# Optimization experiments

Hardware: AMD Instinct MI355X
Metric: run time of the kernel (lower is better)

Reference implementation:

```python
import jax, jax.numpy as jnp
import numpy as np
import math

B, S, HID = 1, 2048, 4096
NH, NKV, HD = 32, 8, 128
ROPE_THETA = 500000.0
NEG = -1e9

def _rope_tables(seq_len, head_dim, theta):
    inv_freq = 1.0 / (theta ** (np.arange(0, head_dim, 2, dtype=np.float32) / head_dim))
    t = np.arange(seq_len, dtype=np.float32)
    freqs = np.outer(t, inv_freq)                      # [S, HD/2]
    emb = np.concatenate([freqs, freqs], axis=-1)      # [S, HD]
    return jnp.asarray(np.cos(emb))[None], jnp.asarray(np.sin(emb))[None]  # [1,S,HD]

def setup_inputs() -> dict:
    key = jax.random.key(0)
    ks = jax.random.split(key, 6)
    hidden_states = jax.random.normal(ks[0], (B, S, HID), jnp.float32)
    # causal additive mask [B,1,S,S]
    causal = jnp.triu(jnp.full((S, S), NEG, jnp.float32), k=1)
    attention_mask = jnp.broadcast_to(causal, (B, 1, S, S))
    cos, sin = _rope_tables(S, HD, ROPE_THETA)
    sc = 0.02
    wq = jax.random.normal(ks[1], (NH * HD, HID), jnp.float32) * sc
    wk = jax.random.normal(ks[2], (NKV * HD, HID), jnp.float32) * sc
    wv = jax.random.normal(ks[3], (NKV * HD, HID), jnp.float32) * sc
    wo = jax.random.normal(ks[4], (HID, NH * HD), jnp.float32) * sc
    return {"hidden_states": hidden_states, "attention_mask": attention_mask,
            "cos": cos, "sin": sin, "wq": wq, "wk": wk, "wv": wv, "wo": wo}

def _rotate_half(x):
    x1, x2 = jnp.split(x, 2, axis=-1)
    return jnp.concatenate([-x2, x1], axis=-1)

def reference(hidden_states, attention_mask, cos, sin, wq, wk, wv, wo):
    b, s, _ = hidden_states.shape
    # QKV projections (torch Linear: x @ W^T)
    q = jnp.einsum('bsm,nm->bsn', hidden_states, wq).reshape(b, s, NH, HD).transpose(0, 2, 1, 3)
    k = jnp.einsum('bsm,nm->bsn', hidden_states, wk).reshape(b, s, NKV, HD).transpose(0, 2, 1, 3)
    v = jnp.einsum('bsm,nm->bsn', hidden_states, wv).reshape(b, s, NKV, HD).transpose(0, 2, 1, 3)
    # RoPE (cos/sin broadcast over heads via unsqueeze dim 1)
    c = cos[:, None, :, :]
    sn = sin[:, None, :, :]
    q = q * c + _rotate_half(q) * sn
    k = k * c + _rotate_half(k) * sn
    # GQA: repeat kv heads
    n_rep = NH // NKV
    k = jnp.repeat(k, n_rep, axis=1)
    v = jnp.repeat(v, n_rep, axis=1)
    scores = jnp.einsum('bhqd,bhkd->bhqk', q, k) / math.sqrt(HD)
    scores = scores + attention_mask[:, :, :, :s]
    attn = jax.nn.softmax(scores.astype(jnp.float32), axis=-1).astype(q.dtype)
    out = jnp.einsum('bhqk,bhkd->bhqd', attn, v)        # [b,NH,s,HD]
    out = out.transpose(0, 2, 1, 3).reshape(b, s, NH * HD)
    return jnp.einsum('bsn,mn->bsm', out, wo)
```

## Files before the change

### kernel.cpp

```cpp
#include <hip/hip_runtime.h>
#include <hip/hip_bf16.h>
#include <stdint.h>

typedef __hip_bfloat16 bf16;
using bf16x8 = __attribute__((ext_vector_type(8))) short;
using f32x4  = __attribute__((ext_vector_type(4))) float;

#define MFMA16(a, b, c) __builtin_amdgcn_mfma_f32_16x16x32_bf16(a, b, c, 0, 0, 0)

#define S_LEN 2048
#define HID   4096
#define NH    32
#define NKV   8
#define HD    128
#define DQ    4096
#define DKV   1024
#define QK_SCALE 0.1275228868824805f

__device__ inline void gl_lds16(const bf16* g, bf16* l) {
    __builtin_amdgcn_global_load_lds(
        (const __attribute__((address_space(1))) void*)g,
        (__attribute__((address_space(3))) void*)l, 16, 0, 0);
}

__device__ inline void cvt_store4(const float* src, bf16* dst, size_t i4) {
    float4 v = ((const float4*)src)[i4];
    union { ushort4 u; bf16 h[4]; } pk;
    pk.h[0] = __float2bfloat16(v.x);
    pk.h[1] = __float2bfloat16(v.y);
    pk.h[2] = __float2bfloat16(v.z);
    pk.h[3] = __float2bfloat16(v.w);
    ((ushort4*)dst)[i4] = pk.u;
}

__global__ void conv_all(const float* __restrict__ hidden, const float* __restrict__ wq,
                         const float* __restrict__ wk, const float* __restrict__ wv,
                         bf16* __restrict__ hb, bf16* __restrict__ wqd,
                         bf16* __restrict__ wkd, bf16* __restrict__ wvd) {
    const size_t M1 = 1024 * 1024;
#pragma unroll
    for (int j = 0; j < 4; ++j) {
        size_t idx = (size_t)blockIdx.x * 1024 + j * 256 + threadIdx.x;
        if (idx < 2 * M1)      cvt_store4(hidden, hb,  idx);
        else if (idx < 6 * M1) cvt_store4(wq,     wqd, idx - 2 * M1);
        else if (idx < 7 * M1) cvt_store4(wk,     wkd, idx - 6 * M1);
        else                   cvt_store4(wv,     wvd, idx - 7 * M1);
    }
}

__global__ void conv_wo(const float* __restrict__ wo, bf16* __restrict__ wod) {
#pragma unroll
    for (int j = 0; j < 4; ++j) {
        size_t idx = (size_t)blockIdx.x * 1024 + j * 256 + threadIdx.x;
        cvt_store4(wo, wod, idx);
    }
}

__global__ void __launch_bounds__(256, 2)
qkv_gemm(const bf16* __restrict__ A, const bf16* __restrict__ Bq,
         const bf16* __restrict__ Bk, const bf16* __restrict__ Bv,
         bf16* __restrict__ Cq, bf16* __restrict__ Ck, bf16* __restrict__ Cv) {
    __shared__ __align__(16) bf16 As[128][64];
    __shared__ __align__(16) bf16 Bs[128][64];

    const int bx = blockIdx.x;
    int mode, bn;
    const bf16* B;
    if (bx < 32)      { mode = 0; B = Bq; bn = bx * 128; }
    else if (bx < 40) { mode = 1; B = Bk; bn = (bx - 32) * 128; }
    else              { mode = 2; B = Bv; bn = (bx - 40) * 128; }

    const int tid  = threadIdx.x;
    const int bm   = blockIdx.y * 128;
    const int wave = tid >> 6, lane = tid & 63;
    const int quad = lane >> 4, l15 = lane & 15;
    const int wr   = (wave >> 1) * 64;
    const int wc   = (wave & 1) * 64;

    f32x4 acc[4][4] = {};

    for (int k0 = 0; k0 < HID; k0 += 64) {
#pragma unroll
        for (int i = 0; i < 4; ++i) {
            int idx  = tid + i * 256;
            int r    = idx >> 3;
            int slot = idx & 7;
            int c    = ((slot - r) & 7) * 8;
            gl_lds16(&A[(size_t)(bm + r) * HID + k0 + c], &As[r][slot * 8]);
            gl_lds16(&B[(size_t)(bn + r) * HID + k0 + c], &Bs[r][slot * 8]);
        }
        __syncthreads();
#pragma unroll
        for (int kk = 0; kk < 64; kk += 32) {
            bf16x8 a[4], b[4];
#pragma unroll
            for (int i = 0; i < 4; ++i) {
                int row = wr + i * 16 + l15;
                a[i] = *(const bf16x8*)(&As[row][(((kk >> 3) + quad + row) & 7) * 8]);
            }
#pragma unroll
            for (int i = 0; i < 4; ++i) {
                int row = wc + i * 16 + l15;
                b[i] = *(const bf16x8*)(&Bs[row][(((kk >> 3) + quad + row) & 7) * 8]);
            }
#pragma unroll
            for (int mi = 0; mi < 4; ++mi)
#pragma unroll
                for (int ni = 0; ni < 4; ++ni)
                    acc[mi][ni] = MFMA16(a[mi], b[ni], acc[mi][ni]);
        }
        __syncthreads();
    }

    if (mode == 0) {
#pragma unroll
        for (int mi = 0; mi < 4; ++mi)
#pragma unroll
            for (int ni = 0; ni < 4; ++ni)
#pragma unroll
                for (int r = 0; r < 4; ++r)
                    Cq[(size_t)(bm + wr + mi * 16 + quad * 4 + r) * DQ +
                       bn + wc + ni * 16 + l15] = __float2bfloat16(acc[mi][ni][r]);
    } else if (mode == 1) {
#pragma unroll
        for (int mi = 0; mi < 4; ++mi)
#pragma unroll
            for (int ni = 0; ni < 4; ++ni)
#pragma unroll
                for (int r = 0; r < 4; ++r)
                    Ck[(size_t)(bm + wr + mi * 16 + quad * 4 + r) * DKV +
                       bn + wc + ni * 16 + l15] = __float2bfloat16(acc[mi][ni][r]);
    } else {
#pragma unroll
        for (int mi = 0; mi < 4; ++mi)
#pragma unroll
            for (int ni = 0; ni < 4; ++ni) {
                int row0 = bm + wr + mi * 16 + quad * 4;
                int col  = bn + wc + ni * 16 + l15;
                union { ushort4 u; bf16 h[4]; } pk;
#pragma unroll
                for (int r = 0; r < 4; ++r) pk.h[r] = __float2bfloat16(acc[mi][ni][r]);
                *(ushort4*)(&Cv[(size_t)col * S_LEN + row0]) = pk.u;
            }
    }
}

__global__ void __launch_bounds__(256, 2)
out_gemm(const bf16* __restrict__ A, const bf16* __restrict__ B,
         float* __restrict__ C) {
    __shared__ __align__(16) bf16 As[128][64];
    __shared__ __align__(16) bf16 Bs[128][64];

    const int tid  = threadIdx.x;
    const int bm   = blockIdx.y * 128;
    const int bn   = blockIdx.x * 128;
    const int wave = tid >> 6, lane = tid & 63;
    const int quad = lane >> 4, l15 = lane & 15;
    const int wr   = (wave >> 1) * 64;
    const int wc   = (wave & 1) * 64;

    f32x4 acc[4][4] = {};

    for (int k0 = 0; k0 < DQ; k0 += 64) {
#pragma unroll
        for (int i = 0; i < 4; ++i) {
            int idx  = tid + i * 256;
            int r    = idx >> 3;
            int slot = idx & 7;
            int c    = ((slot - r) & 7) * 8;
            gl_lds16(&A[(size_t)(bm + r) * DQ + k0 + c], &As[r][slot * 8]);
            gl_lds16(&B[(size_t)(bn + r) * DQ + k0 + c], &Bs[r][slot * 8]);
        }
        __syncthreads();
#pragma unroll
        for (int kk = 0; kk < 64; kk += 32) {
            bf16x8 a[4], b[4];
#pragma unroll
            for (int i = 0; i < 4; ++i) {
                int row = wr + i * 16 + l15;
                a[i] = *(const bf16x8*)(&As[row][(((kk >> 3) + quad + row) & 7) * 8]);
            }
#pragma unroll
            for (int i = 0; i < 4; ++i) {
                int row = wc + i * 16 + l15;
                b[i] = *(const bf16x8*)(&Bs[row][(((kk >> 3) + quad + row) & 7) * 8]);
            }
#pragma unroll
            for (int mi = 0; mi < 4; ++mi)
#pragma unroll
                for (int ni = 0; ni < 4; ++ni)
                    acc[mi][ni] = MFMA16(a[mi], b[ni], acc[mi][ni]);
        }
        __syncthreads();
    }

#pragma unroll
    for (int mi = 0; mi < 4; ++mi)
#pragma unroll
        for (int ni = 0; ni < 4; ++ni)
#pragma unroll
            for (int r = 0; r < 4; ++r)
                C[(size_t)(bm + wr + mi * 16 + quad * 4 + r) * HID +
                  bn + wc + ni * 16 + l15] = acc[mi][ni][r];
}

__global__ void rope_all(bf16* __restrict__ q, bf16* __restrict__ k,
                         const float* __restrict__ cosb, const float* __restrict__ sinb) {
    int idx = blockIdx.x * 256 + threadIdx.x;
    const int nq = S_LEN * NH * 16;
    bf16* x;
    int nheads;
    float mul;
    if (idx < nq) { x = q; nheads = NH; mul = QK_SCALE; }
    else          { x = k; nheads = NKV; mul = 1.0f; idx -= nq; }
    int d4 = (idx & 15) * 4;
    int h  = (idx >> 4) % nheads;
    int s  = idx / (nheads * 16);
    size_t base = (size_t)s * nheads * 128 + (size_t)h * 128 + d4;
    union { ushort4 u; bf16 hh[4]; } i1, i2, o1, o2;
    i1.u = *(const ushort4*)(&x[base]);
    i2.u = *(const ushort4*)(&x[base + 64]);
    float4 c1 = *(const float4*)(&cosb[s * 128 + d4]);
    float4 c2 = *(const float4*)(&cosb[s * 128 + d4 + 64]);
    float4 s1 = *(const float4*)(&sinb[s * 128 + d4]);
    float4 s2 = *(const float4*)(&sinb[s * 128 + d4 + 64]);
#pragma unroll
    for (int j = 0; j < 4; ++j) {
        float x1 = __bfloat162float(i1.hh[j]);
        float x2 = __bfloat162float(i2.hh[j]);
        float cc1 = ((const float*)&c1)[j], cc2 = ((const float*)&c2)[j];
        float ss1 = ((const float*)&s1)[j], ss2 = ((const float*)&s2)[j];
        o1.hh[j] = __float2bfloat16((x1 * cc1 - x2 * ss1) * mul);
        o2.hh[j] = __float2bfloat16((x2 * cc2 + x1 * ss2) * mul);
    }
    *(ushort4*)(&x[base])      = o1.u;
    *(ushort4*)(&x[base + 64]) = o2.u;
}

__device__ __forceinline__ void stage_kv(const bf16* __restrict__ Kp,
                                         const bf16* __restrict__ Vp,
                                         bf16* ks, bf16* vs, int t0, int tid) {
#pragma unroll
    for (int i = 0; i < 4; ++i) {
        int idx = tid + i * 256;
        int t   = idx >> 4;
        int c8  = ((idx & 15) - t) & 15;
        gl_lds16(&Kp[(size_t)(t0 + t) * DKV + c8 * 8], &ks[idx * 8]);
        int d   = idx >> 3;
        int tc  = ((idx & 7) - d) & 7;
        gl_lds16(&Vp[(size_t)d * S_LEN + t0 + tc * 8], &vs[idx * 8]);
    }
}

__global__ void __launch_bounds__(256, 2)
flash_attn(const bf16* Q, const bf16* __restrict__ K,
           const bf16* __restrict__ Vt, bf16* O) {
    __shared__ __align__(16) bf16 Ks[2][64 * 128];
    __shared__ __align__(16) bf16 Vs[2][128 * 64];
    __shared__ __align__(16) bf16 p_lds[4][16][72];

    const int xb   = (int)gridDim.x - 1 - (int)blockIdx.x;
    const int head = blockIdx.y;
    const int kvh  = head >> 2;
    const int tid  = threadIdx.x;
    const int wave = tid >> 6, lane = tid & 63;
    const int quad = lane >> 4, l15 = lane & 15;
    const int q0w  = xb * 64 + wave * 16;

    const bf16* Kp = K + kvh * HD;
    const bf16* Vp = Vt + (size_t)kvh * HD * S_LEN;

    bf16x8 qf[4];
#pragma unroll
    for (int c = 0; c < 4; ++c)
        qf[c] = *(const bf16x8*)(&Q[(size_t)(q0w + l15) * DQ + head * HD + c * 32 + quad * 8]);

    f32x4 o_acc[8] = {};
    float l_part[4] = {0.f, 0.f, 0.f, 0.f};

    const int t_max = (xb + 1) * 64;

    stage_kv(Kp, Vp, &Ks[0][0], &Vs[0][0], 0, tid);
    asm volatile("s_waitcnt vmcnt(0)" ::: "memory");
    __builtin_amdgcn_sched_barrier(0);
    __builtin_amdgcn_s_barrier();
    __builtin_amdgcn_sched_barrier(0);

    int cur = 0;
    for (int t0 = 0; t0 < t_max; t0 += 64) {
        if (t0 + 64 < t_max)
            stage_kv(Kp, Vp, &Ks[cur ^ 1][0], &Vs[cur ^ 1][0], t0 + 64, tid);
        __builtin_amdgcn_sched_barrier(0);

        const bf16* ksb = &Ks[cur][0];
        const bf16* vsb = &Vs[cur][0];

        f32x4 sc[4] = {};
        __builtin_amdgcn_s_setprio(1);
#pragma unroll
        for (int h = 0; h < 4; ++h) {
            int t = h * 16 + l15;
#pragma unroll
            for (int c = 0; c < 4; ++c) {
                bf16x8 kf = *(const bf16x8*)(&ksb[t * 128 + ((c * 4 + quad + t) & 15) * 8]);
                sc[h] = MFMA16(qf[c], kf, sc[h]);
            }
        }
        __builtin_amdgcn_s_setprio(0);

        if (t0 + 64 > q0w) {
#pragma unroll
            for (int r = 0; r < 4; ++r) {
                const int q = q0w + quad * 4 + r;
                float lsum = 0.f;
#pragma unroll
                for (int h = 0; h < 4; ++h) {
                    float a = (t0 + h * 16 + l15 > q) ? -1e30f : sc[h][r];
                    float p = exp2f(a);
                    lsum += p;
                    p_lds[wave][quad * 4 + r][h * 16 + l15] = __float2bfloat16(p);
                }
                l_part[r] += lsum;
            }
        } else {
#pragma unroll
            for (int r = 0; r < 4; ++r) {
                float lsum = 0.f;
#pragma unroll
                for (int h = 0; h < 4; ++h) {
                    float p = exp2f(sc[h][r]);
                    lsum += p;
                    p_lds[wave][quad * 4 + r][h * 16 + l15] = __float2bfloat16(p);
                }
                l_part[r] += lsum;
            }
        }

        asm volatile("" ::: "memory");
        bf16x8 pf0 = *(const bf16x8*)(&p_lds[wave][l15][quad * 8]);
        bf16x8 pf1 = *(const bf16x8*)(&p_lds[wave][l15][32 + quad * 8]);
        __builtin_amdgcn_s_setprio(1);
#pragma unroll
        for (int db = 0; db < 8; ++db) {
            int d = db * 16 + l15;
            bf16x8 vf0 = *(const bf16x8*)(&vsb[d * 64 + ((quad + d) & 7) * 8]);
            bf16x8 vf1 = *(const bf16x8*)(&vsb[d * 64 + ((4 + quad + d) & 7) * 8]);
            o_acc[db] = MFMA16(pf0, vf0, o_acc[db]);
            o_acc[db] = MFMA16(pf1, vf1, o_acc[db]);
        }
        __builtin_amdgcn_s_setprio(0);

        __builtin_amdgcn_sched_barrier(0);
        asm volatile("s_waitcnt vmcnt(0)" ::: "memory");
        __builtin_amdgcn_sched_barrier(0);
        __builtin_amdgcn_s_barrier();
        __builtin_amdgcn_sched_barrier(0);
        cur ^= 1;
    }

#pragma unroll
    for (int r = 0; r < 4; ++r) {
        float l = l_part[r];
        l += __shfl_xor(l, 1);
        l += __shfl_xor(l, 2);
        l += __shfl_xor(l, 4);
        l += __shfl_xor(l, 8);
        float inv = 1.0f / l;
        int row = q0w + quad * 4 + r;
#pragma unroll
        for (int db = 0; db < 8; ++db)
            O[(size_t)row * DQ + head * HD + db * 16 + l15] =
                __float2bfloat16(o_acc[db][r] * inv);
    }
}

extern "C" void kernel_launch(void* const* d_in, const int* in_sizes, int n_in,
                              void* d_out, int out_size, void* d_ws, size_t ws_size,
                              hipStream_t stream) {
    const float* hidden = (const float*)d_in[0];
    const float* cosb   = (const float*)d_in[2];
    const float* sinb   = (const float*)d_in[3];
    const float* wq     = (const float*)d_in[4];
    const float* wk     = (const float*)d_in[5];
    const float* wv     = (const float*)d_in[6];
    const float* wo     = (const float*)d_in[7];
    float* out = (float*)d_out;

    const size_t M1 = 1024 * 1024;
    bf16* hb  = (bf16*)d_ws;
    bf16* wkd = hb + 8 * M1;
    bf16* wvd = hb + 12 * M1;
    bf16* wod = hb;
    bf16* qb  = hb + 16 * M1;
    bf16* kb  = hb + 24 * M1;
    bf16* vt  = hb + 26 * M1;
    bf16* wqd = (bf16*)d_out;

    conv_all<<<8192, 256, 0, stream>>>(hidden, wq, wk, wv, hb, wqd, wkd, wvd);
    qkv_gemm<<<dim3(48, 16), 256, 0, stream>>>(hb, wqd, wkd, wvd, qb, kb, vt);
    conv_wo<<<4096, 256, 0, stream>>>(wo, wod);
    rope_all<<<(S_LEN * (NH + NKV) * 16) / 256, 256, 0, stream>>>(qb, kb, cosb, sinb);
    flash_attn<<<dim3(32, 32), 256, 0, stream>>>(qb, kb, vt, qb);
    out_gemm<<<dim3(32, 16), 256, 0, stream>>>(qb, wod, out);
}
```

Before: 516.5 us.

## Process two 64-row query tiles per flash-attention block to reuse K/V tiles

```diff
diff --git a/kernel.cpp b/kernel.cpp
--- a/kernel.cpp
+++ b/kernel.cpp
@@ -259,26 +259,31 @@
     __shared__ __align__(16) bf16 Vs[2][128 * 64];
     __shared__ __align__(16) bf16 p_lds[4][16][72];
 
-    const int xb   = (int)gridDim.x - 1 - (int)blockIdx.x;
+    const int xb   = blockIdx.x;
     const int head = blockIdx.y;
     const int kvh  = head >> 2;
     const int tid  = threadIdx.x;
     const int wave = tid >> 6, lane = tid & 63;
     const int quad = lane >> 4, l15 = lane & 15;
-    const int q0w  = xb * 64 + wave * 16;
+    const int bq   = xb * 128;
+    const int q0A  = bq + wave * 16;
+    const int q0B  = bq + 64 + wave * 16;
 
     const bf16* Kp = K + kvh * HD;
     const bf16* Vp = Vt + (size_t)kvh * HD * S_LEN;
 
-    bf16x8 qf[4];
-#pragma unroll
-    for (int c = 0; c < 4; ++c)
-        qf[c] = *(const bf16x8*)(&Q[(size_t)(q0w + l15) * DQ + head * HD + c * 32 + quad * 8]);
-
-    f32x4 o_acc[8] = {};
-    float l_part[4] = {0.f, 0.f, 0.f, 0.f};
-
-    const int t_max = (xb + 1) * 64;
+    bf16x8 qfA[4], qfB[4];
+#pragma unroll
+    for (int c = 0; c < 4; ++c) {
+        qfA[c] = *(const bf16x8*)(&Q[(size_t)(q0A + l15) * DQ + head * HD + c * 32 + quad * 8]);
+        qfB[c] = *(const bf16x8*)(&Q[(size_t)(q0B + l15) * DQ + head * HD + c * 32 + quad * 8]);
+    }
+
+    f32x4 oA[8] = {}, oB[8] = {};
+    float lA[4] = {0.f, 0.f, 0.f, 0.f};
+    float lB[4] = {0.f, 0.f, 0.f, 0.f};
+
+    const int t_end = bq + 128;
 
     stage_kv(Kp, Vp, &Ks[0][0], &Vs[0][0], 0, tid);
     asm volatile("s_waitcnt vmcnt(0)" ::: "memory");
@@ -287,15 +292,16 @@
     __builtin_amdgcn_sched_barrier(0);
 
     int cur = 0;
-    for (int t0 = 0; t0 < t_max; t0 += 64) {
-        if (t0 + 64 < t_max)
+    for (int t0 = 0; t0 < t_end; t0 += 64) {
+        if (t0 + 64 < t_end)
             stage_kv(Kp, Vp, &Ks[cur ^ 1][0], &Vs[cur ^ 1][0], t0 + 64, tid);
         __builtin_amdgcn_sched_barrier(0);
 
         const bf16* ksb = &Ks[cur][0];
         const bf16* vsb = &Vs[cur][0];
-
-        f32x4 sc[4] = {};
+        const bool actA = (t0 <= bq);
+
+        f32x4 scA[4] = {}, scB[4] = {};
         __builtin_amdgcn_s_setprio(1);
 #pragma unroll
         for (int h = 0; h < 4; ++h) {
@@ -303,24 +309,60 @@
 #pragma unroll
             for (int c = 0; c < 4; ++c) {
                 bf16x8 kf = *(const bf16x8*)(&ksb[t * 128 + ((c * 4 + quad + t) & 15) * 8]);
-                sc[h] = MFMA16(qf[c], kf, sc[h]);
+                if (actA) scA[h] = MFMA16(qfA[c], kf, scA[h]);
+                scB[h] = MFMA16(qfB[c], kf, scB[h]);
             }
         }
         __builtin_amdgcn_s_setprio(0);
 
-        if (t0 + 64 > q0w) {
+        bf16x8 pfA0 = {}, pfA1 = {};
+        if (actA) {
+            if (t0 + 64 > q0A) {
+#pragma unroll
+                for (int r = 0; r < 4; ++r) {
+                    const int q = q0A + quad * 4 + r;
+                    float lsum = 0.f;
+#pragma unroll
+                    for (int h = 0; h < 4; ++h) {
+                        float a = (t0 + h * 16 + l15 > q) ? -1e30f : scA[h][r];
+                        float p = exp2f(a);
+                        lsum += p;
+                        p_lds[wave][quad * 4 + r][h * 16 + l15] = __float2bfloat16(p);
+                    }
+                    lA[r] += lsum;
+                }
+            } else {
+#pragma unroll
+                for (int r = 0; r < 4; ++r) {
+                    float lsum = 0.f;
+#pragma unroll
+                    for (int h = 0; h < 4; ++h) {
+                        float p = exp2f(scA[h][r]);
+                        lsum += p;
+                        p_lds[wave][quad * 4 + r][h * 16 + l15] = __float2bfloat16(p);
+                    }
+                    lA[r] += lsum;
+                }
+            }
+            asm volatile("" ::: "memory");
+            pfA0 = *(const bf16x8*)(&p_lds[wave][l15][quad * 8]);
+            pfA1 = *(const bf16x8*)(&p_lds[wave][l15][32 + quad * 8]);
+            asm volatile("" ::: "memory");
+        }
+
+        if (t0 + 64 > q0B) {
 #pragma unroll
             for (int r = 0; r < 4; ++r) {
-                const int q = q0w + quad * 4 + r;
+                const int q = q0B + quad * 4 + r;
                 float lsum = 0.f;
 #pragma unroll
                 for (int h = 0; h < 4; ++h) {
-                    float a = (t0 + h * 16 + l15 > q) ? -1e30f : sc[h][r];
+                    float a = (t0 + h * 16 + l15 > q) ? -1e30f : scB[h][r];
                     float p = exp2f(a);
                     lsum += p;
                     p_lds[wave][quad * 4 + r][h * 16 + l15] = __float2bfloat16(p);
                 }
-                l_part[r] += lsum;
+                lB[r] += lsum;
             }
         } else {
 #pragma unroll
@@ -328,25 +370,29 @@
                 float lsum = 0.f;
 #pragma unroll
                 for (int h = 0; h < 4; ++h) {
-                    float p = exp2f(sc[h][r]);
+                    float p = exp2f(scB[h][r]);
                     lsum += p;
                     p_lds[wave][quad * 4 + r][h * 16 + l15] = __float2bfloat16(p);
                 }
-                l_part[r] += lsum;
-            }
-        }
-
+                lB[r] += lsum;
+            }
+        }
         asm volatile("" ::: "memory");
-        bf16x8 pf0 = *(const bf16x8*)(&p_lds[wave][l15][quad * 8]);
-        bf16x8 pf1 = *(const bf16x8*)(&p_lds[wave][l15][32 + quad * 8]);
+        bf16x8 pfB0 = *(const bf16x8*)(&p_lds[wave][l15][quad * 8]);
+        bf16x8 pfB1 = *(const bf16x8*)(&p_lds[wave][l15][32 + quad * 8]);
+
         __builtin_amdgcn_s_setprio(1);
 #pragma unroll
         for (int db = 0; db < 8; ++db) {
             int d = db * 16 + l15;
             bf16x8 vf0 = *(const bf16x8*)(&vsb[d * 64 + ((quad + d) & 7) * 8]);
             bf16x8 vf1 = *(const bf16x8*)(&vsb[d * 64 + ((4 + quad + d) & 7) * 8]);
-            o_acc[db] = MFMA16(pf0, vf0, o_acc[db]);
-            o_acc[db] = MFMA16(pf1, vf1, o_acc[db]);
+            if (actA) {
+                oA[db] = MFMA16(pfA0, vf0, oA[db]);
+                oA[db] = MFMA16(pfA1, vf1, oA[db]);
+            }
+            oB[db] = MFMA16(pfB0, vf0, oB[db]);
+            oB[db] = MFMA16(pfB1, vf1, oB[db]);
         }
         __builtin_amdgcn_s_setprio(0);
 
@@ -360,17 +406,29 @@
 
 #pragma unroll
     for (int r = 0; r < 4; ++r) {
-        float l = l_part[r];
-        l += __shfl_xor(l, 1);
-        l += __shfl_xor(l, 2);
-        l += __shfl_xor(l, 4);
-        l += __shfl_xor(l, 8);
-        float inv = 1.0f / l;
-        int row = q0w + quad * 4 + r;
+        float la = lA[r];
+        la += __shfl_xor(la, 1);
+        la += __shfl_xor(la, 2);
+        la += __shfl_xor(la, 4);
+        la += __shfl_xor(la, 8);
+        float inva = 1.0f / la;
+        int rowa = q0A + quad * 4 + r;
 #pragma unroll
         for (int db = 0; db < 8; ++db)
-            O[(size_t)row * DQ + head * HD + db * 16 + l15] =
-                __float2bfloat16(o_acc[db][r] * inv);
+            O[(size_t)rowa * DQ + head * HD + db * 16 + l15] =
+                __float2bfloat16(oA[db][r] * inva);
+
+        float lb = lB[r];
+        lb += __shfl_xor(lb, 1);
+        lb += __shfl_xor(lb, 2);
+        lb += __shfl_xor(lb, 4);
+        lb += __shfl_xor(lb, 8);
+        float invb = 1.0f / lb;
+        int rowb = q0B + quad * 4 + r;
+#pragma unroll
+        for (int db = 0; db < 8; ++db)
+            O[(size_t)rowb * DQ + head * HD + db * 16 + l15] =
+                __float2bfloat16(oB[db][r] * invb);
     }
 }
 
@@ -400,6 +458,6 @@
     qkv_gemm<<<dim3(48, 16), 256, 0, stream>>>(hb, wqd, wkd, wvd, qb, kb, vt);
     conv_wo<<<4096, 256, 0, stream>>>(wo, wod);
     rope_all<<<(S_LEN * (NH + NKV) * 16) / 256, 256, 0, stream>>>(qb, kb, cosb, sinb);
-    flash_attn<<<dim3(32, 32), 256, 0, stream>>>(qb, kb, vt, qb);
+    flash_attn<<<dim3(16, 32), 256, 0, stream>>>(qb, kb, vt, qb);
     out_gemm<<<dim3(32, 16), 256, 0, stream>>>(qb, wod, out);
 }
```

Result: no change. 518.3 us (+0.4%).
